# Kernel tuning notes

Hardware: AMD Instinct MI355X
Metric: run time of the kernel (lower is better)

The kernel has to match this reference:

```python
import jax, jax.numpy as jnp
import numpy as np

N_NODES = 100000
N_EDGES = 1600000
IN_FEATS = 64
OUT_FEATS = 32


def setup_inputs() -> dict:
    key = jax.random.key(0)
    k_h, k_src, k_dst, k_ord, k_w, k_b = jax.random.split(key, 6)
    stdv = 1.0 / np.sqrt(OUT_FEATS)
    return {
        "h": jax.random.normal(k_h, (N_NODES, IN_FEATS), dtype=jnp.float32),
        "src": jax.random.randint(k_src, (N_EDGES,), 0, N_NODES),
        "dst": jax.random.randint(k_dst, (N_EDGES,), 0, N_NODES),
        "edge_order": jax.random.uniform(k_ord, (N_EDGES,), dtype=jnp.float32),
        "W": jax.random.uniform(k_w, (IN_FEATS, OUT_FEATS), dtype=jnp.float32, minval=-stdv, maxval=stdv),
        "b": jax.random.uniform(k_b, (OUT_FEATS,), dtype=jnp.float32, minval=-stdv, maxval=stdv),
    }


def reference(h, src, dst, edge_order, W, b):
    # dropout p=0.0 -> disabled (self.dropout is falsy in the original)
    h = h @ W                                      # [N, out_feats]
    # message: per-edge scalar 'order' * source features, summed at dst
    msg = edge_order[:, None] * h[src]             # [E, out_feats]
    agg = jax.ops.segment_sum(msg, dst, num_segments=N_NODES)
    # self.norm is None != 'none' -> norm branch taken; not 'both' -> 1/deg
    degs = jax.ops.segment_sum(jnp.ones_like(edge_order), dst, num_segments=N_NODES)
    norm = 1.0 / jnp.clip(degs, 1.0)               # [N]
    out = agg * norm[:, None] + b
    return jax.nn.relu(out)
```

## Files before the change

### kernel.cpp

```cpp
#include <hip/hip_runtime.h>


constexpr int N_NODES = 100000;
constexpr int N_EDGES = 1600000;
constexpr int IN_F    = 64;
constexpr int OUT_F   = 32;
constexpr int SHIFT   = 6;
constexpr int NPB     = 1 << SHIFT;
constexpr int NB      = (N_NODES + NPB - 1) >> SHIFT;
constexpr int PCHUNK  = 3200;
constexpr int PBLOCKS = N_EDGES / PCHUNK;
constexpr int CBLOCKS = 128;
constexpr int CE      = N_EDGES / CBLOCKS;
constexpr int SCAP    = 2048;

__global__ __launch_bounds__(256) void gemm64x32_zero(const float* __restrict__ h,
                                                      const float* __restrict__ W,
                                                      float* __restrict__ hw,
                                                      int* __restrict__ binTot) {
    __shared__ float Ws[IN_F * OUT_F];
    __shared__ float hs[8 * IN_F];
    const int tid = threadIdx.x;

    #pragma unroll
    for (int i = tid; i < IN_F * OUT_F; i += 256) Ws[i] = W[i];

    const int rowBase = blockIdx.x * 8;
    ((float2*)hs)[tid] = ((const float2*)(h + (size_t)rowBase * IN_F))[tid];

    for (int i = blockIdx.x * 256 + tid; i < NB; i += gridDim.x * 256) binTot[i] = 0;

    __syncthreads();

    const int rl = tid >> 5;
    const int f  = tid & 31;
    float sum = 0.f;
    #pragma unroll
    for (int k = 0; k < IN_F; ++k)
        sum = fmaf(hs[rl * IN_F + k], Ws[k * OUT_F + f], sum);

    hw[(size_t)rowBase * OUT_F + tid] = sum;
}

__global__ __launch_bounds__(256) void k_count(const int* __restrict__ dst,
                                               int* __restrict__ binTot) {
    __shared__ int hist[NB];
    const int tid = threadIdx.x;
    for (int i = tid; i < NB; i += 256) hist[i] = 0;
    __syncthreads();
    const int base = blockIdx.x * CE;
    for (int j = tid; j < CE; j += 256)
        atomicAdd(&hist[dst[base + j] >> SHIFT], 1);
    __syncthreads();
    for (int c = tid; c < NB; c += 256) {
        const int v = hist[c];
        if (v) atomicAdd(&binTot[c], v);
    }
}

__global__ __launch_bounds__(256) void k_scan(const int* __restrict__ binTot,
                                              int* __restrict__ binStart,
                                              int* __restrict__ cursor) {
    __shared__ int wt[4];
    const int tid = threadIdx.x, lane = tid & 63, wid = tid >> 6;
    const int base = tid * 8;
    int loc[8]; int run = 0;
    #pragma unroll
    for (int j = 0; j < 8; ++j) {
        const int i = base + j;
        const int c = (i < NB) ? binTot[i] : 0;
        loc[j] = run; run += c;
    }
    int s = run;
    #pragma unroll
    for (int d = 1; d < 64; d <<= 1) { const int t = __shfl_up(s, d); if (lane >= d) s += t; }
    if (lane == 63) wt[wid] = s;
    __syncthreads();
    int wex = 0;
    for (int w = 0; w < wid; ++w) wex += wt[w];
    const int tex = wex + s - run;
    #pragma unroll
    for (int j = 0; j < 8; ++j) {
        const int i = base + j;
        if (i < NB) { const int e = tex + loc[j]; binStart[i] = e; cursor[i] = e; }
    }
}

__global__ __launch_bounds__(256, 2) void k_part(const int* __restrict__ src,
                                                 const int* __restrict__ dst,
                                                 const float* __restrict__ ord,
                                                 int* __restrict__ cursor,
                                                 unsigned long long* __restrict__ coarse) {
    __shared__ unsigned long long sorted[PCHUNK];
    __shared__ unsigned short    binOf[PCHUNK];
    __shared__ int hist[NB];
    __shared__ int rnk[NB];
    __shared__ int gbase[NB];
    __shared__ int sEx[NB];
    __shared__ int wt[4];
    const int tid = threadIdx.x, lane = tid & 63, wid = tid >> 6;
    const int ebase = blockIdx.x * PCHUNK;

    for (int i = tid; i < NB; i += 256) { hist[i] = 0; rnk[i] = 0; }
    __syncthreads();

    for (int j = tid; j < PCHUNK; j += 256)
        atomicAdd(&hist[dst[ebase + j] >> SHIFT], 1);
    __syncthreads();

    {
        const int base = tid * 8;
        int loc[8]; int run = 0;
        #pragma unroll
        for (int j = 0; j < 8; ++j) {
            const int i = base + j;
            const int c = (i < NB) ? hist[i] : 0;
            loc[j] = run; run += c;
        }
        int s = run;
        #pragma unroll
        for (int d = 1; d < 64; d <<= 1) { const int t = __shfl_up(s, d); if (lane >= d) s += t; }
        if (lane == 63) wt[wid] = s;
        __syncthreads();
        int wex = 0;
        for (int w = 0; w < wid; ++w) wex += wt[w];
        const int tex = wex + s - run;
        #pragma unroll
        for (int j = 0; j < 8; ++j) {
            const int i = base + j;
            if (i < NB) sEx[i] = tex + loc[j];
        }
    }
    __syncthreads();

    for (int c = tid; c < NB; c += 256) {
        const int h = hist[c];
        if (h) gbase[c] = atomicAdd(&cursor[c], h);
    }

    for (int j = tid; j < PCHUNK; j += 256) {
        const int e  = ebase + j;
        const int d_ = dst[e];
        const int c  = d_ >> SHIFT;
        const int r  = atomicAdd(&rnk[c], 1);
        const int slot = sEx[c] + r;
        sorted[slot] = ((unsigned long long)__float_as_uint(ord[e]) << 32) |
                       ((unsigned int)src[e] << SHIFT) | (unsigned int)(d_ & (NPB - 1));
        binOf[slot]  = (unsigned short)c;
    }
    __syncthreads();

    for (int i = tid; i < PCHUNK; i += 256) {
        const int c = binOf[i];
        coarse[(size_t)(gbase[c] + (i - sEx[c]))] = sorted[i];
    }
}

__global__ __launch_bounds__(256, 4) void k_sort(unsigned long long* __restrict__ coarse,
                                                 const int* __restrict__ binStart,
                                                 const int* __restrict__ binTot,
                                                 int* __restrict__ nodeStart,
                                                 int* __restrict__ nodeCnt) {
    __shared__ unsigned long long pay[SCAP];
    __shared__ unsigned long long pay2[SCAP];
    __shared__ int cnt[NPB];
    __shared__ int cur[NPB];
    const int tid   = threadIdx.x;
    const int b     = blockIdx.x;
    const int start = binStart[b];
    const int tot   = binTot[b];

    if (tid < NPB) cnt[tid] = 0;
    __syncthreads();

    for (int i = tid; i < tot; i += 256) {
        const unsigned long long p = coarse[(size_t)start + i];
        pay[i] = p;
        atomicAdd(&cnt[(unsigned)p & (NPB - 1)], 1);
    }
    __syncthreads();

    if (tid < 64) {
        const int c = cnt[tid];
        int s = c;
        #pragma unroll
        for (int d = 1; d < 64; d <<= 1) { const int t = __shfl_up(s, d); if (tid >= d) s += t; }
        const int ex = s - c;
        cur[tid] = ex;
        nodeStart[b * NPB + tid] = start + ex;
        nodeCnt [b * NPB + tid] = c;
    }
    __syncthreads();

    for (int i = tid; i < tot; i += 256) {
        const unsigned long long p = pay[i];
        const int r = atomicAdd(&cur[(unsigned)p & (NPB - 1)], 1);
        pay2[r] = p;
    }
    __syncthreads();

    for (int i = tid; i < tot; i += 256)
        coarse[(size_t)start + i] = pay2[i];
}

__global__ __launch_bounds__(256, 8) void k_gather2(const unsigned long long* __restrict__ coarse,
                                                    const int* __restrict__ nodeStart,
                                                    const int* __restrict__ nodeCnt,
                                                    const float* __restrict__ hw,
                                                    const float* __restrict__ bias,
                                                    float* __restrict__ out) {
    const int i = blockIdx.x * 256 + threadIdx.x;
    const int n = i >> 3;
    const int q = i & 7;

    const int st = nodeStart[n];
    const int dg = nodeCnt[n];

    float4 acc = make_float4(0.f, 0.f, 0.f, 0.f);
    for (int j = 0; j < dg; ++j) {
        const unsigned long long p = coarse[(size_t)st + j];
        const float o = __uint_as_float((unsigned)(p >> 32));
        const int   s = (int)(((unsigned)p) >> SHIFT);
        const float4 v = *(const float4*)(hw + (size_t)s * OUT_F + q * 4);
        acc.x = fmaf(o, v.x, acc.x);
        acc.y = fmaf(o, v.y, acc.y);
        acc.z = fmaf(o, v.z, acc.z);
        acc.w = fmaf(o, v.w, acc.w);
    }

    const float norm = 1.0f / fmaxf((float)dg, 1.0f);
    const float4 bb  = *(const float4*)(bias + q * 4);
    float4 r;
    r.x = fmaxf(fmaf(acc.x, norm, bb.x), 0.f);
    r.y = fmaxf(fmaf(acc.y, norm, bb.y), 0.f);
    r.z = fmaxf(fmaf(acc.z, norm, bb.z), 0.f);
    r.w = fmaxf(fmaf(acc.w, norm, bb.w), 0.f);
    *(float4*)(out + (size_t)n * OUT_F + q * 4) = r;
}

extern "C" void kernel_launch(void* const* d_in, const int* in_sizes, int n_in,
                              void* d_out, int out_size, void* d_ws, size_t ws_size,
                              hipStream_t stream) {
    const float* h   = (const float*)d_in[0];
    const int*   src = (const int*)  d_in[1];
    const int*   dst = (const int*)  d_in[2];
    const float* ord = (const float*)d_in[3];
    const float* W   = (const float*)d_in[4];
    const float* b   = (const float*)d_in[5];
    float*       out = (float*)d_out;

    unsigned long long* coarse = (unsigned long long*)d_ws;
    float* hw        = (float*)(coarse + N_EDGES);
    int*   binTot    = (int*)(hw + (size_t)N_NODES * OUT_F);
    int*   binStart  = binTot + NB;
    int*   cursor    = binStart + NB;
    int*   nodeStart = cursor + NB;
    int*   nodeCnt   = nodeStart + NB * NPB;

    hipLaunchKernelGGL(gemm64x32_zero, dim3(N_NODES / 8), dim3(256), 0, stream,
                       h, W, hw, binTot);
    hipLaunchKernelGGL(k_count, dim3(CBLOCKS), dim3(256), 0, stream, dst, binTot);
    hipLaunchKernelGGL(k_scan, dim3(1), dim3(256), 0, stream,
                       binTot, binStart, cursor);
    hipLaunchKernelGGL(k_part, dim3(PBLOCKS), dim3(256), 0, stream,
                       src, dst, ord, cursor, coarse);
    hipLaunchKernelGGL(k_sort, dim3(NB), dim3(256), 0, stream,
                       coarse, binStart, binTot, nodeStart, nodeCnt);
    hipLaunchKernelGGL(k_gather2, dim3(N_NODES * 8 / 256), dim3(256), 0, stream,
                       coarse, nodeStart, nodeCnt, hw, b, out);
}
```

Before: 229.0 us.

## Widen partition/sort blocks and unroll gather loop by four

Partition and sort kernels move to 512-thread blocks with adjusted launch bounds, and the partition prefix scan is changed to four bins per thread to match. Count kernel block count doubles. The gather loop is unrolled by four so several edge payloads and feature loads are in flight at once, and its occupancy hint drops to 6. The aim is more memory-level parallelism and better latency hiding. The cost is more registers per thread and possible shared-memory-limited occupancy for k_part.

```diff
diff --git a/kernel.cpp b/kernel.cpp
--- a/kernel.cpp
+++ b/kernel.cpp
@@ -10,7 +10,8 @@
 constexpr int NB      = (N_NODES + NPB - 1) >> SHIFT;
 constexpr int PCHUNK  = 3200;
 constexpr int PBLOCKS = N_EDGES / PCHUNK;
-constexpr int CBLOCKS = 128;
+constexpr int PTH     = 512;
+constexpr int CBLOCKS = 256;
 constexpr int CE      = N_EDGES / CBLOCKS;
 constexpr int SCAP    = 2048;
 
@@ -86,7 +87,7 @@
     }
 }
 
-__global__ __launch_bounds__(256, 2) void k_part(const int* __restrict__ src,
+__global__ __launch_bounds__(PTH, 4) void k_part(const int* __restrict__ src,
                                                  const int* __restrict__ dst,
                                                  const float* __restrict__ ord,
                                                  int* __restrict__ cursor,
@@ -97,22 +98,22 @@
     __shared__ int rnk[NB];
     __shared__ int gbase[NB];
     __shared__ int sEx[NB];
-    __shared__ int wt[4];
+    __shared__ int wt[PTH / 64];
     const int tid = threadIdx.x, lane = tid & 63, wid = tid >> 6;
     const int ebase = blockIdx.x * PCHUNK;
 
-    for (int i = tid; i < NB; i += 256) { hist[i] = 0; rnk[i] = 0; }
-    __syncthreads();
-
-    for (int j = tid; j < PCHUNK; j += 256)
+    for (int i = tid; i < NB; i += PTH) { hist[i] = 0; rnk[i] = 0; }
+    __syncthreads();
+
+    for (int j = tid; j < PCHUNK; j += PTH)
         atomicAdd(&hist[dst[ebase + j] >> SHIFT], 1);
     __syncthreads();
 
     {
-        const int base = tid * 8;
-        int loc[8]; int run = 0;
-        #pragma unroll
-        for (int j = 0; j < 8; ++j) {
+        const int base = tid * 4;
+        int loc[4]; int run = 0;
+        #pragma unroll
+        for (int j = 0; j < 4; ++j) {
             const int i = base + j;
             const int c = (i < NB) ? hist[i] : 0;
             loc[j] = run; run += c;
@@ -126,19 +127,19 @@
         for (int w = 0; w < wid; ++w) wex += wt[w];
         const int tex = wex + s - run;
         #pragma unroll
-        for (int j = 0; j < 8; ++j) {
+        for (int j = 0; j < 4; ++j) {
             const int i = base + j;
             if (i < NB) sEx[i] = tex + loc[j];
         }
     }
     __syncthreads();
 
-    for (int c = tid; c < NB; c += 256) {
+    for (int c = tid; c < NB; c += PTH) {
         const int h = hist[c];
         if (h) gbase[c] = atomicAdd(&cursor[c], h);
     }
 
-    for (int j = tid; j < PCHUNK; j += 256) {
+    for (int j = tid; j < PCHUNK; j += PTH) {
         const int e  = ebase + j;
         const int d_ = dst[e];
         const int c  = d_ >> SHIFT;
@@ -150,13 +151,13 @@
     }
     __syncthreads();
 
-    for (int i = tid; i < PCHUNK; i += 256) {
+    for (int i = tid; i < PCHUNK; i += PTH) {
         const int c = binOf[i];
         coarse[(size_t)(gbase[c] + (i - sEx[c]))] = sorted[i];
     }
 }
 
-__global__ __launch_bounds__(256, 4) void k_sort(unsigned long long* __restrict__ coarse,
+__global__ __launch_bounds__(512, 8) void k_sort(unsigned long long* __restrict__ coarse,
                                                  const int* __restrict__ binStart,
                                                  const int* __restrict__ binTot,
                                                  int* __restrict__ nodeStart,
@@ -173,7 +174,7 @@
     if (tid < NPB) cnt[tid] = 0;
     __syncthreads();
 
-    for (int i = tid; i < tot; i += 256) {
+    for (int i = tid; i < tot; i += 512) {
         const unsigned long long p = coarse[(size_t)start + i];
         pay[i] = p;
         atomicAdd(&cnt[(unsigned)p & (NPB - 1)], 1);
@@ -192,18 +193,18 @@
     }
     __syncthreads();
 
-    for (int i = tid; i < tot; i += 256) {
+    for (int i = tid; i < tot; i += 512) {
         const unsigned long long p = pay[i];
         const int r = atomicAdd(&cur[(unsigned)p & (NPB - 1)], 1);
         pay2[r] = p;
     }
     __syncthreads();
 
-    for (int i = tid; i < tot; i += 256)
+    for (int i = tid; i < tot; i += 512)
         coarse[(size_t)start + i] = pay2[i];
 }
 
-__global__ __launch_bounds__(256, 8) void k_gather2(const unsigned long long* __restrict__ coarse,
+__global__ __launch_bounds__(256, 6) void k_gather2(const unsigned long long* __restrict__ coarse,
                                                     const int* __restrict__ nodeStart,
                                                     const int* __restrict__ nodeCnt,
                                                     const float* __restrict__ hw,
@@ -217,11 +218,34 @@
     const int dg = nodeCnt[n];
 
     float4 acc = make_float4(0.f, 0.f, 0.f, 0.f);
-    for (int j = 0; j < dg; ++j) {
+    const int full = dg & ~3;
+    int j = 0;
+    for (; j < full; j += 4) {
+        const unsigned long long p0 = coarse[(size_t)st + j + 0];
+        const unsigned long long p1 = coarse[(size_t)st + j + 1];
+        const unsigned long long p2 = coarse[(size_t)st + j + 2];
+        const unsigned long long p3 = coarse[(size_t)st + j + 3];
+        const float4 v0 = *(const float4*)(hw + (size_t)(((unsigned)p0) >> SHIFT) * OUT_F + q * 4);
+        const float4 v1 = *(const float4*)(hw + (size_t)(((unsigned)p1) >> SHIFT) * OUT_F + q * 4);
+        const float4 v2 = *(const float4*)(hw + (size_t)(((unsigned)p2) >> SHIFT) * OUT_F + q * 4);
+        const float4 v3 = *(const float4*)(hw + (size_t)(((unsigned)p3) >> SHIFT) * OUT_F + q * 4);
+        const float o0 = __uint_as_float((unsigned)(p0 >> 32));
+        const float o1 = __uint_as_float((unsigned)(p1 >> 32));
+        const float o2 = __uint_as_float((unsigned)(p2 >> 32));
+        const float o3 = __uint_as_float((unsigned)(p3 >> 32));
+        acc.x = fmaf(o0, v0.x, acc.x); acc.y = fmaf(o0, v0.y, acc.y);
+        acc.z = fmaf(o0, v0.z, acc.z); acc.w = fmaf(o0, v0.w, acc.w);
+        acc.x = fmaf(o1, v1.x, acc.x); acc.y = fmaf(o1, v1.y, acc.y);
+        acc.z = fmaf(o1, v1.z, acc.z); acc.w = fmaf(o1, v1.w, acc.w);
+        acc.x = fmaf(o2, v2.x, acc.x); acc.y = fmaf(o2, v2.y, acc.y);
+        acc.z = fmaf(o2, v2.z, acc.z); acc.w = fmaf(o2, v2.w, acc.w);
+        acc.x = fmaf(o3, v3.x, acc.x); acc.y = fmaf(o3, v3.y, acc.y);
+        acc.z = fmaf(o3, v3.z, acc.z); acc.w = fmaf(o3, v3.w, acc.w);
+    }
+    for (; j < dg; ++j) {
         const unsigned long long p = coarse[(size_t)st + j];
         const float o = __uint_as_float((unsigned)(p >> 32));
-        const int   s = (int)(((unsigned)p) >> SHIFT);
-        const float4 v = *(const float4*)(hw + (size_t)s * OUT_F + q * 4);
+        const float4 v = *(const float4*)(hw + (size_t)(((unsigned)p) >> SHIFT) * OUT_F + q * 4);
         acc.x = fmaf(o, v.x, acc.x);
         acc.y = fmaf(o, v.y, acc.y);
         acc.z = fmaf(o, v.z, acc.z);
@@ -262,9 +286,9 @@
     hipLaunchKernelGGL(k_count, dim3(CBLOCKS), dim3(256), 0, stream, dst, binTot);
     hipLaunchKernelGGL(k_scan, dim3(1), dim3(256), 0, stream,
                        binTot, binStart, cursor);
-    hipLaunchKernelGGL(k_part, dim3(PBLOCKS), dim3(256), 0, stream,
+    hipLaunchKernelGGL(k_part, dim3(PBLOCKS), dim3(PTH), 0, stream,
                        src, dst, ord, cursor, coarse);
-    hipLaunchKernelGGL(k_sort, dim3(NB), dim3(256), 0, stream,
+    hipLaunchKernelGGL(k_sort, dim3(NB), dim3(512), 0, stream,
                        coarse, binStart, binTot, nodeStart, nodeCnt);
     hipLaunchKernelGGL(k_gather2, dim3(N_NODES * 8 / 256), dim3(256), 0, stream,
                        coarse, nodeStart, nodeCnt, hw, b, out);
```

Result: faster. 211.7 us (-7.5%).
